# Kernel tuning notes

Hardware: AMD Instinct MI355X
Metric: run time of the kernel (lower is better)

Reference implementation:

```python
import jax, jax.numpy as jnp
import numpy as np

WS, SHIFT, HEADS, FEAT = 7, 3, 3, 56
N = WS * WS

def _rel_pos_index(ws):
    coords = np.stack(np.meshgrid(np.arange(ws), np.arange(ws), indexing='ij'))  # 2,ws,ws
    coords = coords.reshape(2, -1)
    rel = coords[:, :, None] - coords[:, None, :]            # 2,N,N
    rel = rel.transpose(1, 2, 0).astype(np.int64)            # N,N,2
    rel[:, :, 0] += ws - 1
    rel[:, :, 1] += ws - 1
    rel[:, :, 0] *= 2 * ws - 1
    return rel.sum(-1)                                       # N,N in [0,(2ws-1)^2)

def _shift_mask(H, ws, shift):
    img = np.zeros((H, H), dtype=np.float32)
    cnt = 0
    for hs in (slice(0, -ws), slice(-ws, -shift), slice(-shift, None)):
        for wl in (slice(0, -ws), slice(-ws, -shift), slice(-shift, None)):
            img[hs, wl] = cnt
            cnt += 1
    win = img.reshape(H // ws, ws, H // ws, ws).transpose(0, 2, 1, 3).reshape(-1, ws * ws)
    diff = win[:, None, :] - win[:, :, None]                 # nW,N,N (unsqueeze(1)-unsqueeze(2))
    return np.where(diff != 0, -100.0, 0.0).astype(np.float32)

_REL_IDX = jnp.asarray(_rel_pos_index(WS))
_MASK = jnp.asarray(_shift_mask(FEAT, WS, SHIFT))            # (nW_per_img, N, N)

def setup_inputs() -> dict:
    key = jax.random.key(0)
    ks = jax.random.split(key, 4)
    C = 96
    return {
        'x': jax.random.normal(ks[0], (128, C, FEAT, FEAT), jnp.float32),
        'ln_g': jnp.ones((C,), jnp.float32),
        'ln_b': jnp.zeros((C,), jnp.float32),
        'qkv_w': jax.random.normal(ks[1], (3 * C, C), jnp.float32) * 0.02,
        'qkv_b': jnp.zeros((3 * C,), jnp.float32),
        'proj_w': jax.random.normal(ks[2], (C, C), jnp.float32) * 0.02,
        'proj_b': jnp.zeros((C,), jnp.float32),
        'rel_table': jax.random.normal(ks[3], ((2 * WS - 1) ** 2, HEADS), jnp.float32) * 0.02,
    }

def reference(x, ln_g, ln_b, qkv_w, qkv_b, proj_w, proj_b, rel_table):
    B, C, H, W = x.shape
    hd = C // HEADS
    nwh = H // WS
    # BCHW -> BHWC, LayerNorm over C
    xt = x.transpose(0, 2, 3, 1)
    mu = xt.mean(-1, keepdims=True)
    var = ((xt - mu) ** 2).mean(-1, keepdims=True)
    xn = (xt - mu) * jax.lax.rsqrt(var + 1e-5) * ln_g + ln_b
    # cyclic shift
    xn = jnp.roll(xn, (-SHIFT, -SHIFT), axis=(1, 2))
    # window partition -> (B*nW, N, C)
    win = xn.reshape(B, nwh, WS, nwh, WS, C).transpose(0, 1, 3, 2, 4, 5).reshape(-1, N, C)
    # qkv
    qkv = (win @ qkv_w.T + qkv_b).reshape(-1, N, 3, HEADS, hd).transpose(2, 0, 3, 1, 4)
    q, k, v = qkv[0], qkv[1], qkv[2]                         # (B*nW, heads, N, hd)
    attn = jnp.einsum('whid,whjd->whij', q * (hd ** -0.5), k)
    bias = rel_table[_REL_IDX].transpose(2, 0, 1)            # heads,N,N
    attn = attn + bias[None]
    nWp = nwh * nwh
    attn = attn.reshape(B, nWp, HEADS, N, N) + _MASK[None, :, None]
    attn = jax.nn.softmax(attn, axis=-1).reshape(-1, HEADS, N, N)
    out = jnp.einsum('whij,whjd->whid', attn, v).transpose(0, 2, 1, 3).reshape(-1, N, C)
    out = out @ proj_w.T + proj_b
    # window reverse + unshift
    out = out.reshape(B, nwh, nwh, WS, WS, C).transpose(0, 1, 3, 2, 4, 5).reshape(B, H, W, C)
    out = jnp.roll(out, (SHIFT, SHIFT), axis=(1, 2))
    return out.transpose(0, 3, 1, 2)
```

## Files before the change

kernel.cpp:

```cpp
#include <hip/hip_runtime.h>

typedef unsigned short u16;
typedef __bf16 bf8v __attribute__((ext_vector_type(8)));
typedef float f4v __attribute__((ext_vector_type(4)));
typedef f4v __attribute__((may_alias)) f4va;
typedef unsigned int u2v __attribute__((ext_vector_type(2)));
typedef u2v __attribute__((may_alias)) u2va;
typedef unsigned int u4v __attribute__((ext_vector_type(4)));
typedef u4v __attribute__((may_alias)) u4va;

#define NTOK   49
#define NPAD   64
#define CDIM   96
#define FEAT_  56
#define HWIM   3136
#define SHIFT_ 3

#define WIN_ELEMS (128 * 64 * 49 * 96)
#define QW_ELEMS  (288 * 96)
#define PW_ELEMS  (96 * 96)
#define WS_NEEDED ((size_t)(WIN_ELEMS + QW_ELEMS + PW_ELEMS) * 2)

__device__ __forceinline__ float b2f(u16 u) {
  unsigned v = ((unsigned)u) << 16;
  return __builtin_bit_cast(float, v);
}
__device__ __forceinline__ u16 f2b(float f) {
  return __builtin_bit_cast(u16, (__bf16)f);
}
__device__ __forceinline__ unsigned pk2(float a, float b) {
  return (unsigned)f2b(a) | ((unsigned)f2b(b) << 16);
}
__device__ __forceinline__ bf8v fragld(const u16* p) {
  return __builtin_bit_cast(bf8v, *(const f4va*)p);
}
__device__ __forceinline__ bf8v cvt8(const float* p) {
  f4v a = *(const f4va*)p;
  f4v b = *(const f4va*)(p + 4);
  union { u16 u[8]; bf8v v; } r;
#pragma unroll
  for (int j = 0; j < 4; ++j) { r.u[j] = f2b(a[j]); r.u[4 + j] = f2b(b[j]); }
  return r.v;
}
__device__ __forceinline__ f4v mfma16(bf8v a, bf8v b, f4v c) {
  return __builtin_amdgcn_mfma_f32_16x16x32_bf16(a, b, c, 0, 0, 0);
}
__device__ __forceinline__ int reg3(int g) { return g < 49 ? 0 : (g < 53 ? 1 : 2); }

__global__ __launch_bounds__(256)
void swin_wcvt(const float* __restrict__ qw, const float* __restrict__ pw,
               u16* __restrict__ qwb, u16* __restrict__ pwb) {
  int i = blockIdx.x * 256 + threadIdx.x;
  if (i < QW_ELEMS) qwb[i] = f2b(qw[i]);
  else              pwb[i - QW_ELEMS] = f2b(pw[i - QW_ELEMS]);
}

__global__ __launch_bounds__(256, 6)
void swin_ln_pack(const float* __restrict__ x,
                  const float* __restrict__ lng, const float* __restrict__ lnb,
                  u16* __restrict__ winbuf) {
  __shared__ __align__(16) float xf[CDIM][60];
  __shared__ float ps[4][64], pq[4][64];
  __shared__ float gw[CDIM], bw[CDIM];

  const int bid = blockIdx.x;
  const int b = bid / FEAT_, hs = bid - b * FEAT_;
  int h = hs + SHIFT_; if (h >= FEAT_) h -= FEAT_;
  const int tid = threadIdx.x, wv = tid >> 6, lane = tid & 63;

  for (int i = tid; i < CDIM; i += 256) { gw[i] = lng[i]; bw[i] = lnb[i]; }

  const float* base = x + (size_t)b * CDIM * HWIM + h * FEAT_;
  for (int idx = tid; idx < 1344; idx += 256) {
    int c = idx / 14, p4 = idx - c * 14;
    *(f4va*)&xf[c][p4 * 4] = *(const f4va*)(base + (size_t)c * HWIM + p4 * 4);
  }
  __syncthreads();

  const int ws = lane;
  int wsrc = ws + SHIFT_; if (wsrc >= FEAT_) wsrc -= FEAT_;
  float s = 0.f, q = 0.f;
  if (ws < FEAT_)
    for (int i = 0; i < 24; ++i) {
      float v = xf[wv * 24 + i][wsrc];
      s += v; q += v * v;
    }
  ps[wv][lane] = s; pq[wv][lane] = q;
  __syncthreads();

  if (ws < FEAT_) {
    float ts = ps[0][ws] + ps[1][ws] + ps[2][ws] + ps[3][ws];
    float tq = pq[0][ws] + pq[1][ws] + pq[2][ws] + pq[3][ws];
    float m = ts * (1.f / 96.f);
    float r = rsqrtf(tq * (1.f / 96.f) - m * m + 1e-5f);
    const int ww = ws / 7, wl = ws - ww * 7;
    const int wrow = hs / 7, tr = hs - wrow * 7;
    u16* dst = winbuf + ((size_t)((b * 64 + wrow * 8 + ww) * 49 + tr * 7 + wl)) * CDIM + wv * 24;
    unsigned pkw[12];
#pragma unroll
    for (int i = 0; i < 12; ++i) {
      int c = wv * 24 + 2 * i;
      float v0 = (xf[c][wsrc] - m) * r * gw[c] + bw[c];
      float v1 = (xf[c + 1][wsrc] - m) * r * gw[c + 1] + bw[c + 1];
      pkw[i] = pk2(v0, v1);
    }
    u4v d0 = {pkw[0], pkw[1], pkw[2], pkw[3]};
    u4v d1 = {pkw[4], pkw[5], pkw[6], pkw[7]};
    u4v d2 = {pkw[8], pkw[9], pkw[10], pkw[11]};
    *(u4va*)(dst)      = d0;
    *(u4va*)(dst + 8)  = d1;
    *(u4va*)(dst + 16) = d2;
  }
}

__global__ __launch_bounds__(256, 3)
void swin_attn(u16* __restrict__ winbuf,
               const u16* __restrict__ qwb, const u16* __restrict__ pwb,
               const float* __restrict__ qbv, const float* __restrict__ pbv,
               const float* __restrict__ rel) {
  __shared__ __align__(16) u16 qk[NPAD][200];
  __shared__ __align__(16) u16 vt[3][32][72];
  __shared__ __align__(16) u16 Pl[NPAD][72];
  __shared__ float rel_f[507];
  __shared__ __align__(16) float pb_f[CDIM];
  __shared__ __align__(16) float qb_f[3 * CDIM];

  const int blk = blockIdx.x;
  const int wi = blk & 63;
  const int whb = wi >> 3, wwb = wi & 7;
  const int tid = threadIdx.x;
  const int wv = tid >> 6, lane = tid & 63;
  const int quad = lane >> 4, l15 = lane & 15;

  u16* wbase = winbuf + (size_t)blk * (NTOK * CDIM);

  for (int idx = tid; idx < 588; idx += 256) {
    int row = idx / 12, cc = idx - row * 12;
    *(f4va*)&qk[row][cc * 8] = *(const f4va*)(wbase + idx * 8);
  }
  {
    f4v z = {0.f, 0.f, 0.f, 0.f};
    for (int idx = tid; idx < 180; idx += 256) {
      int row = 49 + idx / 12, cc = idx - (idx / 12) * 12;
      *(f4va*)&qk[row][cc * 8] = z;
    }
  }
  for (int i = tid; i < 507; i += 256) rel_f[i] = rel[i];
  for (int i = tid; i < 3 * CDIM; i += 256) qb_f[i] = qbv[i];
  for (int i = tid; i < CDIM; i += 256) pb_f[i] = pbv[i];
  __syncthreads();

  {
    bf8v a[4][3];
#pragma unroll
    for (int mt = 0; mt < 4; ++mt)
#pragma unroll
      for (int kt = 0; kt < 3; ++kt)
        a[mt][kt] = fragld(&qk[mt * 16 + l15][kt * 32 + quad * 8]);
    __syncthreads();
    const float qscale = 0.17677669529663687f;
    for (int nt = wv; nt < 18; nt += 4) {
      int n = nt * 16 + l15;
      bf8v bf[3];
#pragma unroll
      for (int kt = 0; kt < 3; ++kt)
        bf[kt] = fragld(qwb + n * CDIM + kt * 32 + quad * 8);
      if (nt < 12) {
        const int n0 = nt * 16 + quad * 4;
        f4v bias = *(const f4va*)&qb_f[n0];
        const bool isq = (nt < 6);
#pragma unroll
        for (int mt = 0; mt < 4; ++mt) {
          f4v c = {0.f, 0.f, 0.f, 0.f};
          c = mfma16(bf[0], a[mt][0], c);
          c = mfma16(bf[1], a[mt][1], c);
          c = mfma16(bf[2], a[mt][2], c);
          float v0 = c[0] + bias[0], v1 = c[1] + bias[1];
          float v2 = c[2] + bias[2], v3 = c[3] + bias[3];
          if (isq) { v0 *= qscale; v1 *= qscale; v2 *= qscale; v3 *= qscale; }
          u2v d; d[0] = pk2(v0, v1); d[1] = pk2(v2, v3);
          *(u2va*)&qk[mt * 16 + l15][n0] = d;
        }
      } else {
        float bias = qb_f[n];
        const int hd = (n - 192) >> 5, dc = (n - 192) & 31;
#pragma unroll
        for (int mt = 0; mt < 4; ++mt) {
          f4v c = {0.f, 0.f, 0.f, 0.f};
          c = mfma16(a[mt][0], bf[0], c);
          c = mfma16(a[mt][1], bf[1], c);
          c = mfma16(a[mt][2], bf[2], c);
          u2v d; d[0] = pk2(c[0] + bias, c[1] + bias);
          d[1] = pk2(c[2] + bias, c[3] + bias);
          *(u2va*)&vt[hd][dc][mt * 16 + quad * 4] = d;
        }
      }
    }
  }
  __syncthreads();

  {
    const int mrow = wv * 16 + l15;
    int mc = mrow > 48 ? 48 : mrow;
    const int ri = mc / 7, ci = mc - ri * 7;
    const int rcnt = reg3(whb * 7 + ri) * 3 + reg3(wwb * 7 + ci);
    int ib_[4][4]; float ms_[4][4]; bool jv_[4][4];
#pragma unroll
    for (int jt = 0; jt < 4; ++jt)
#pragma unroll
      for (int rg = 0; rg < 4; ++rg) {
        int j = jt * 16 + quad * 4 + rg;
        jv_[jt][rg] = (j < NTOK);
        int jj = j > 48 ? 48 : j;
        int rj = jj / 7, cj = jj - rj * 7;
        int jcnt = reg3(whb * 7 + rj) * 3 + reg3(wwb * 7 + cj);
        ib_[jt][rg] = ((ri - rj + 6) * 13 + (ci - cj + 6)) * 3;
        ms_[jt][rg] = (jcnt != rcnt) ? -100.f : 0.f;
      }
#pragma unroll
    for (int h = 0; h < 3; ++h) {
      bf8v aq = fragld(&qk[wv * 16 + l15][h * 32 + quad * 8]);
      f4v S[4];
#pragma unroll
      for (int jt = 0; jt < 4; ++jt) {
        bf8v bk = fragld(&qk[jt * 16 + l15][96 + h * 32 + quad * 8]);
        f4v z = {0.f, 0.f, 0.f, 0.f};
        S[jt] = mfma16(bk, aq, z);
      }
#pragma unroll
      for (int jt = 0; jt < 4; ++jt)
#pragma unroll
        for (int rg = 0; rg < 4; ++rg) {
          if (jv_[jt][rg]) S[jt][rg] += rel_f[ib_[jt][rg] + h] + ms_[jt][rg];
          else             S[jt][rg] = -1e30f;
        }
      float mx0 = fmaxf(fmaxf(S[0][0], S[0][1]), fmaxf(S[0][2], S[0][3]));
      float mx1 = fmaxf(fmaxf(S[1][0], S[1][1]), fmaxf(S[1][2], S[1][3]));
      float mx2 = fmaxf(fmaxf(S[2][0], S[2][1]), fmaxf(S[2][2], S[2][3]));
      float mx3 = fmaxf(fmaxf(S[3][0], S[3][1]), fmaxf(S[3][2], S[3][3]));
      float mx = fmaxf(fmaxf(mx0, mx1), fmaxf(mx2, mx3));
      mx = fmaxf(mx, __shfl_xor(mx, 16, 64));
      mx = fmaxf(mx, __shfl_xor(mx, 32, 64));
      float s = 0.f;
#pragma unroll
      for (int jt = 0; jt < 4; ++jt) {
        float e0 = __expf(S[jt][0] - mx), e1 = __expf(S[jt][1] - mx);
        float e2 = __expf(S[jt][2] - mx), e3 = __expf(S[jt][3] - mx);
        S[jt][0] = e0; S[jt][1] = e1; S[jt][2] = e2; S[jt][3] = e3;
        s += (e0 + e1) + (e2 + e3);
      }
      s += __shfl_xor(s, 16, 64);
      s += __shfl_xor(s, 32, 64);
      float inv = 1.f / s;
#pragma unroll
      for (int jt = 0; jt < 4; ++jt) {
        u2v d; d[0] = pk2(S[jt][0] * inv, S[jt][1] * inv);
        d[1] = pk2(S[jt][2] * inv, S[jt][3] * inv);
        *(u2va*)&Pl[mrow][jt * 16 + quad * 4] = d;
      }
      bf8v ap0 = fragld(&Pl[wv * 16 + l15][quad * 8]);
      bf8v ap1 = fragld(&Pl[wv * 16 + l15][32 + quad * 8]);
#pragma unroll
      for (int dt = 0; dt < 2; ++dt) {
        bf8v bv0 = fragld(&vt[h][dt * 16 + l15][quad * 8]);
        bf8v bv1 = fragld(&vt[h][dt * 16 + l15][32 + quad * 8]);
        f4v c = {0.f, 0.f, 0.f, 0.f};
        c = mfma16(bv0, ap0, c);
        c = mfma16(bv1, ap1, c);
        u2v d; d[0] = pk2(c[0], c[1]); d[1] = pk2(c[2], c[3]);
        *(u2va*)&qk[mrow][h * 32 + dt * 16 + quad * 4] = d;
      }
    }
  }
  __syncthreads();

  {
    bf8v a[4][3];
#pragma unroll
    for (int mt = 0; mt < 4; ++mt)
#pragma unroll
      for (int kt = 0; kt < 3; ++kt)
        a[mt][kt] = fragld(&qk[mt * 16 + l15][kt * 32 + quad * 8]);
    __syncthreads();
    for (int nt = wv; nt < 6; nt += 4) {
      int n = nt * 16 + l15;
      bf8v bf[3];
#pragma unroll
      for (int kt = 0; kt < 3; ++kt)
        bf[kt] = fragld(pwb + n * CDIM + kt * 32 + quad * 8);
      const int n0 = nt * 16 + quad * 4;
      f4v bias = *(const f4va*)&pb_f[n0];
#pragma unroll
      for (int mt = 0; mt < 4; ++mt) {
        f4v c = {0.f, 0.f, 0.f, 0.f};
        c = mfma16(bf[0], a[mt][0], c);
        c = mfma16(bf[1], a[mt][1], c);
        c = mfma16(bf[2], a[mt][2], c);
        u2v d; d[0] = pk2(c[0] + bias[0], c[1] + bias[1]);
        d[1] = pk2(c[2] + bias[2], c[3] + bias[3]);
        *(u2va*)&qk[mt * 16 + l15][n0] = d;
      }
    }
  }
  __syncthreads();

  for (int idx = tid; idx < 588; idx += 256) {
    int row = idx / 12, cc = idx - row * 12;
    *(f4va*)(wbase + idx * 8) = *(const f4va*)&qk[row][cc * 8];
  }
}

__global__ __launch_bounds__(256, 8)
void swin_unpack(const u16* __restrict__ winbuf, float* __restrict__ out) {
  __shared__ __align__(16) u16 wtile[64][104];
  const int bid = blockIdx.x;
  const int b = bid / FEAT_, h = bid - b * FEAT_;
  int hs = h - SHIFT_; if (hs < 0) hs += FEAT_;
  const int wrow = hs / 7, tr = hs - wrow * 7;
  const int tid = threadIdx.x, wv = tid >> 6, lane = tid & 63;

  for (int idx = tid; idx < 672; idx += 256) {
    int ww = idx / 84, r = idx - ww * 84;
    const u16* src = winbuf + ((size_t)((b * 64 + wrow * 8 + ww) * 49 + tr * 7)) * CDIM + r * 8;
    int wl = r / 12, cc = r - wl * 12;
    int ws = ww * 7 + wl;
    int w = ws + SHIFT_; if (w >= FEAT_) w -= FEAT_;
    int sr = (w >> 2) | ((w & 3) << 4);
    *(f4va*)&wtile[sr][cc * 8] = *(const f4va*)src;
  }
  __syncthreads();
  if (lane < 56) {
    const int g = lane / 14, p4 = lane - g * 14;
    float* obase = out + (size_t)b * CDIM * HWIM + h * FEAT_ + p4 * 4;
    for (int i = 0; i < 6; ++i) {
      int c = wv * 24 + i * 4 + g;
      f4v v;
#pragma unroll
      for (int j = 0; j < 4; ++j) v[j] = b2f(wtile[p4 + 16 * j][c]);
      *(f4va*)(obase + (size_t)c * HWIM) = v;
    }
  }
}

__global__ __launch_bounds__(256, 2)
void swin_fused_fb(const float* __restrict__ x,
                   const float* __restrict__ lng, const float* __restrict__ lnb,
                   const float* __restrict__ qw,  const float* __restrict__ qbv,
                   const float* __restrict__ pw,  const float* __restrict__ pbv,
                   const float* __restrict__ rel,
                   float* __restrict__ out) {
  __shared__ union { float xf[NTOK][97]; u16 qk[NPAD][200]; } A;
  __shared__ union { u16 win16[NPAD][104]; u16 outb[NPAD][98]; } Bu;
  __shared__ u16 vt[3][32][72];
  __shared__ u16 Pl[NPAD][72];
  __shared__ u16 att[NPAD][104];
  __shared__ float gw[CDIM], bwt[CDIM];
  __shared__ float rel_f[507];
  __shared__ float pb_f[CDIM];
  __shared__ float qb_f[3 * CDIM];

  const int blk = blockIdx.x;
  const int b = blk >> 6, wi = blk & 63;
  const int whb = wi >> 3, wwb = wi & 7;
  const int tid = threadIdx.x, wv = tid >> 6, lane = tid & 63;
  const int quad = lane >> 4, l15 = lane & 15;
  {
    int p = lane;
    if (p < NTOK) {
      int r = p / 7, cw = p - r * 7;
      int h = whb * 7 + r + SHIFT_;  if (h >= FEAT_) h -= FEAT_;
      int w = wwb * 7 + cw + SHIFT_; if (w >= FEAT_) w -= FEAT_;
      const float* xp = x + b * CDIM * HWIM + h * FEAT_ + w;
      for (int c = wv; c < CDIM; c += 4) A.xf[p][c] = xp[c * HWIM];
    }
    for (int i = tid; i < CDIM; i += 256) { gw[i] = lng[i]; bwt[i] = lnb[i]; pb_f[i] = pbv[i]; }
    for (int i = tid; i < 507; i += 256) rel_f[i] = rel[i];
    for (int i = tid; i < 3 * CDIM; i += 256) qb_f[i] = qbv[i];
  }
  __syncthreads();
  {
    int p = wv * 16 + (lane >> 2), cg = lane & 3;
    float s = 0.f, q = 0.f;
    if (p < NTOK)
      for (int i = 0; i < 24; ++i) { float v = A.xf[p][cg * 24 + i]; s += v; q += v * v; }
    s += __shfl_xor(s, 1, 64); s += __shfl_xor(s, 2, 64);
    q += __shfl_xor(q, 1, 64); q += __shfl_xor(q, 2, 64);
    float m = s * (1.f / 96.f);
    float r = rsqrtf(q * (1.f / 96.f) - m * m + 1e-5f);
    for (int i = 0; i < 24; ++i) {
      int c = cg * 24 + i;
      float v = (p < NTOK) ? (A.xf[p][c] - m) * r * gw[c] + bwt[c] : 0.f;
      Bu.win16[p][c] = f2b(v);
    }
  }
  __syncthreads();
  {
    bf8v a[4][3];
    for (int mt = 0; mt < 4; ++mt)
      for (int kt = 0; kt < 3; ++kt)
        a[mt][kt] = fragld(&Bu.win16[mt * 16 + l15][kt * 32 + quad * 8]);
    const float qscale = 0.17677669529663687f;
    for (int nt = wv; nt < 18; nt += 4) {
      int n = nt * 16 + l15;
      const float* wr = qw + n * CDIM;
      bf8v bf[3];
      for (int kt = 0; kt < 3; ++kt) bf[kt] = cvt8(wr + kt * 32 + quad * 8);
      float bias = qb_f[n];
      for (int mt = 0; mt < 4; ++mt) {
        f4v c = {0.f, 0.f, 0.f, 0.f};
        c = mfma16(a[mt][0], bf[0], c);
        c = mfma16(a[mt][1], bf[1], c);
        c = mfma16(a[mt][2], bf[2], c);
        for (int rg = 0; rg < 4; ++rg) {
          int m = mt * 16 + quad * 4 + rg;
          float v = c[rg] + bias;
          if (n < 96)        A.qk[m][n] = f2b(v * qscale);
          else if (n < 192)  A.qk[m][n] = f2b(v);
          else               vt[(n - 192) >> 5][(n - 192) & 31][m] = f2b(v);
        }
      }
    }
  }
  __syncthreads();
  {
    const int rbase = wv * 16 + quad * 4;
    int rcnt[4], ri_[4], ci_[4];
    for (int rg = 0; rg < 4; ++rg) {
      int r = rbase + rg; if (r > 48) r = 48;
      int ri = r / 7, ci = r - ri * 7;
      ri_[rg] = ri; ci_[rg] = ci;
      rcnt[rg] = reg3(whb * 7 + ri) * 3 + reg3(wwb * 7 + ci);
    }
    for (int h = 0; h < 3; ++h) {
      bf8v aq = fragld(&A.qk[wv * 16 + l15][h * 32 + quad * 8]);
      f4v S[4];
      for (int nt = 0; nt < 4; ++nt) {
        bf8v bk = fragld(&A.qk[nt * 16 + l15][96 + h * 32 + quad * 8]);
        f4v z = {0.f, 0.f, 0.f, 0.f};
        S[nt] = mfma16(aq, bk, z);
      }
      for (int nt = 0; nt < 4; ++nt) {
        int j = nt * 16 + l15;
        if (j < NTOK) {
          int rj = j / 7, cj = j - rj * 7;
          int jcnt = reg3(whb * 7 + rj) * 3 + reg3(wwb * 7 + cj);
          for (int rg = 0; rg < 4; ++rg) {
            float add = rel_f[((ri_[rg] - rj + 6) * 13 + (ci_[rg] - cj + 6)) * 3 + h];
            if (jcnt != rcnt[rg]) add -= 100.f;
            S[nt][rg] += add;
          }
        } else {
          for (int rg = 0; rg < 4; ++rg) S[nt][rg] = -1e30f;
        }
      }
      float inv[4];
      for (int rg = 0; rg < 4; ++rg) {
        float m = fmaxf(fmaxf(S[0][rg], S[1][rg]), fmaxf(S[2][rg], S[3][rg]));
        for (int off = 1; off < 16; off <<= 1) m = fmaxf(m, __shfl_xor(m, off, 64));
        float s = 0.f;
        for (int nt = 0; nt < 4; ++nt) { float e = __expf(S[nt][rg] - m); S[nt][rg] = e; s += e; }
        for (int off = 1; off < 16; off <<= 1) s += __shfl_xor(s, off, 64);
        inv[rg] = 1.f / s;
      }
      for (int nt = 0; nt < 4; ++nt) {
        int j = nt * 16 + l15;
        for (int rg = 0; rg < 4; ++rg) Pl[rbase + rg][j] = f2b(S[nt][rg] * inv[rg]);
      }
      bf8v ap0 = fragld(&Pl[wv * 16 + l15][quad * 8]);
      bf8v ap1 = fragld(&Pl[wv * 16 + l15][32 + quad * 8]);
      for (int nt = 0; nt < 2; ++nt) {
        bf8v bv0 = fragld(&vt[h][nt * 16 + l15][quad * 8]);
        bf8v bv1 = fragld(&vt[h][nt * 16 + l15][32 + quad * 8]);
        f4v c = {0.f, 0.f, 0.f, 0.f};
        c = mfma16(ap0, bv0, c);
        c = mfma16(ap1, bv1, c);
        for (int rg = 0; rg < 4; ++rg)
          att[rbase + rg][h * 32 + nt * 16 + l15] = f2b(c[rg]);
      }
    }
  }
  __syncthreads();
  {
    bf8v a[4][3];
    for (int mt = 0; mt < 4; ++mt)
      for (int kt = 0; kt < 3; ++kt)
        a[mt][kt] = fragld(&att[mt * 16 + l15][kt * 32 + quad * 8]);
    for (int nt = wv; nt < 6; nt += 4) {
      int n = nt * 16 + l15;
      const float* wr = pw + n * CDIM;
      bf8v bf[3];
      for (int kt = 0; kt < 3; ++kt) bf[kt] = cvt8(wr + kt * 32 + quad * 8);
      float bias = pb_f[n];
      for (int mt = 0; mt < 4; ++mt) {
        f4v c = {0.f, 0.f, 0.f, 0.f};
        c = mfma16(a[mt][0], bf[0], c);
        c = mfma16(a[mt][1], bf[1], c);
        c = mfma16(a[mt][2], bf[2], c);
        for (int rg = 0; rg < 4; ++rg)
          Bu.outb[mt * 16 + quad * 4 + rg][n] = f2b(c[rg] + bias);
      }
    }
  }
  __syncthreads();
  {
    int p = lane;
    if (p < NTOK) {
      int r = p / 7, cw = p - r * 7;
      int h = whb * 7 + r + SHIFT_;  if (h >= FEAT_) h -= FEAT_;
      int w = wwb * 7 + cw + SHIFT_; if (w >= FEAT_) w -= FEAT_;
      float* op = out + b * CDIM * HWIM + h * FEAT_ + w;
      for (int c = wv; c < CDIM; c += 4) op[c * HWIM] = b2f(Bu.outb[p][c]);
    }
  }
}

extern "C" void kernel_launch(void* const* d_in, const int* in_sizes, int n_in,
                              void* d_out, int out_size, void* d_ws, size_t ws_size,
                              hipStream_t stream) {
  (void)in_sizes; (void)n_in; (void)out_size;
  const float* x   = (const float*)d_in[0];
  const float* lng = (const float*)d_in[1];
  const float* lnb = (const float*)d_in[2];
  const float* qw  = (const float*)d_in[3];
  const float* qbv = (const float*)d_in[4];
  const float* pw  = (const float*)d_in[5];
  const float* pbv = (const float*)d_in[6];
  const float* rel = (const float*)d_in[7];
  float* out = (float*)d_out;

  if (ws_size >= WS_NEEDED) {
    u16* winbuf = (u16*)d_ws;
    u16* qwb = winbuf + WIN_ELEMS;
    u16* pwb = qwb + QW_ELEMS;
    swin_wcvt<<<dim3(144), dim3(256), 0, stream>>>(qw, pw, qwb, pwb);
    swin_ln_pack<<<dim3(128 * FEAT_), dim3(256), 0, stream>>>(x, lng, lnb, winbuf);
    swin_attn<<<dim3(8192), dim3(256), 0, stream>>>(winbuf, qwb, pwb, qbv, pbv, rel);
    swin_unpack<<<dim3(128 * FEAT_), dim3(256), 0, stream>>>(winbuf, out);
  } else {
    swin_fused_fb<<<dim3(8192), dim3(256), 0, stream>>>(x, lng, lnb, qw, qbv, pw, pbv, rel, out);
  }
}
```

Baseline: 447.7 us.

## Fuse layernorm pack, window attention and unpack into one kernel

```diff
diff --git a/kernel.cpp b/kernel.cpp
--- a/kernel.cpp
+++ b/kernel.cpp
@@ -16,10 +16,9 @@
 #define HWIM   3136
 #define SHIFT_ 3
 
-#define WIN_ELEMS (128 * 64 * 49 * 96)
 #define QW_ELEMS  (288 * 96)
 #define PW_ELEMS  (96 * 96)
-#define WS_NEEDED ((size_t)(WIN_ELEMS + QW_ELEMS + PW_ELEMS) * 2)
+#define WS_NEEDED ((size_t)(QW_ELEMS + PW_ELEMS) * 2)
 
 __device__ __forceinline__ float b2f(u16 u) {
   unsigned v = ((unsigned)u) << 16;
@@ -55,99 +54,77 @@
   else              pwb[i - QW_ELEMS] = f2b(pw[i - QW_ELEMS]);
 }
 
-__global__ __launch_bounds__(256, 6)
-void swin_ln_pack(const float* __restrict__ x,
-                  const float* __restrict__ lng, const float* __restrict__ lnb,
-                  u16* __restrict__ winbuf) {
-  __shared__ __align__(16) float xf[CDIM][60];
-  __shared__ float ps[4][64], pq[4][64];
+__global__ __launch_bounds__(256, 3)
+void swin_mono(const float* __restrict__ x,
+               const float* __restrict__ lng, const float* __restrict__ lnb,
+               const u16* __restrict__ qwb, const u16* __restrict__ pwb,
+               const float* __restrict__ qbv, const float* __restrict__ pbv,
+               const float* __restrict__ rel, float* __restrict__ out) {
+  __shared__ __align__(16) u16 qk[NPAD][200];
+  __shared__ __align__(16) union {
+    struct { u16 vt[3][32][72]; u16 Pl[NPAD][72]; } s;
+    float xf[NTOK][97];
+  } U;
+  __shared__ float rel_f[507];
+  __shared__ __align__(16) float pb_f[CDIM];
+  __shared__ __align__(16) float qb_f[3 * CDIM];
   __shared__ float gw[CDIM], bw[CDIM];
 
   const int bid = blockIdx.x;
-  const int b = bid / FEAT_, hs = bid - b * FEAT_;
-  int h = hs + SHIFT_; if (h >= FEAT_) h -= FEAT_;
-  const int tid = threadIdx.x, wv = tid >> 6, lane = tid & 63;
-
-  for (int i = tid; i < CDIM; i += 256) { gw[i] = lng[i]; bw[i] = lnb[i]; }
-
-  const float* base = x + (size_t)b * CDIM * HWIM + h * FEAT_;
-  for (int idx = tid; idx < 1344; idx += 256) {
-    int c = idx / 14, p4 = idx - c * 14;
-    *(f4va*)&xf[c][p4 * 4] = *(const f4va*)(base + (size_t)c * HWIM + p4 * 4);
-  }
-  __syncthreads();
-
-  const int ws = lane;
-  int wsrc = ws + SHIFT_; if (wsrc >= FEAT_) wsrc -= FEAT_;
-  float s = 0.f, q = 0.f;
-  if (ws < FEAT_)
-    for (int i = 0; i < 24; ++i) {
-      float v = xf[wv * 24 + i][wsrc];
-      s += v; q += v * v;
-    }
-  ps[wv][lane] = s; pq[wv][lane] = q;
-  __syncthreads();
-
-  if (ws < FEAT_) {
-    float ts = ps[0][ws] + ps[1][ws] + ps[2][ws] + ps[3][ws];
-    float tq = pq[0][ws] + pq[1][ws] + pq[2][ws] + pq[3][ws];
-    float m = ts * (1.f / 96.f);
-    float r = rsqrtf(tq * (1.f / 96.f) - m * m + 1e-5f);
-    const int ww = ws / 7, wl = ws - ww * 7;
-    const int wrow = hs / 7, tr = hs - wrow * 7;
-    u16* dst = winbuf + ((size_t)((b * 64 + wrow * 8 + ww) * 49 + tr * 7 + wl)) * CDIM + wv * 24;
+  const int wwb = bid >> 10;
+  const int b = (bid >> 3) & 127;
+  const int whb = bid & 7;
+  const int tid = threadIdx.x;
+  const int wv = tid >> 6, lane = tid & 63;
+  const int quad = lane >> 4, l15 = lane & 15;
+
+  for (int i = tid; i < 507; i += 256) rel_f[i] = rel[i];
+  for (int i = tid; i < 3 * CDIM; i += 256) qb_f[i] = qbv[i];
+  for (int i = tid; i < CDIM; i += 256) { pb_f[i] = pbv[i]; gw[i] = lng[i]; bw[i] = lnb[i]; }
+
+  const int w0 = wwb * 7 + SHIFT_;
+  for (int idx = tid; idx < 672; idx += 256) {
+    int r = idx / 96, c = idx - r * 96;
+    int hsrc = whb * 7 + r + SHIFT_; if (hsrc >= FEAT_) hsrc -= FEAT_;
+    const float* xp = x + ((size_t)b * CDIM + c) * HWIM + hsrc * FEAT_;
+#pragma unroll
+    for (int wl = 0; wl < 7; ++wl) {
+      int wsrc = w0 + wl; if (wsrc >= FEAT_) wsrc -= FEAT_;
+      U.xf[r * 7 + wl][c] = xp[wsrc];
+    }
+  }
+  __syncthreads();
+
+  {
+    const int p = tid >> 2, cg = tid & 3;
+    const float* xr = U.xf[p < NTOK ? p : 0];
+    float s = 0.f, q = 0.f;
+    if (p < NTOK)
+#pragma unroll
+      for (int i = 0; i < 24; ++i) { float v = xr[cg * 24 + i]; s += v; q += v * v; }
+    s += __shfl_xor(s, 1, 64); s += __shfl_xor(s, 2, 64);
+    q += __shfl_xor(q, 1, 64); q += __shfl_xor(q, 2, 64);
+    float m = s * (1.f / 96.f);
+    float r = rsqrtf(q * (1.f / 96.f) - m * m + 1e-5f);
     unsigned pkw[12];
 #pragma unroll
     for (int i = 0; i < 12; ++i) {
-      int c = wv * 24 + 2 * i;
-      float v0 = (xf[c][wsrc] - m) * r * gw[c] + bw[c];
-      float v1 = (xf[c + 1][wsrc] - m) * r * gw[c + 1] + bw[c + 1];
+      int c0 = cg * 24 + 2 * i;
+      float v0 = 0.f, v1 = 0.f;
+      if (p < NTOK) {
+        v0 = (xr[c0] - m) * r * gw[c0] + bw[c0];
+        v1 = (xr[c0 + 1] - m) * r * gw[c0 + 1] + bw[c0 + 1];
+      }
       pkw[i] = pk2(v0, v1);
     }
     u4v d0 = {pkw[0], pkw[1], pkw[2], pkw[3]};
     u4v d1 = {pkw[4], pkw[5], pkw[6], pkw[7]};
     u4v d2 = {pkw[8], pkw[9], pkw[10], pkw[11]};
+    u16* dst = &qk[p][cg * 24];
     *(u4va*)(dst)      = d0;
     *(u4va*)(dst + 8)  = d1;
     *(u4va*)(dst + 16) = d2;
   }
-}
-
-__global__ __launch_bounds__(256, 3)
-void swin_attn(u16* __restrict__ winbuf,
-               const u16* __restrict__ qwb, const u16* __restrict__ pwb,
-               const float* __restrict__ qbv, const float* __restrict__ pbv,
-               const float* __restrict__ rel) {
-  __shared__ __align__(16) u16 qk[NPAD][200];
-  __shared__ __align__(16) u16 vt[3][32][72];
-  __shared__ __align__(16) u16 Pl[NPAD][72];
-  __shared__ float rel_f[507];
-  __shared__ __align__(16) float pb_f[CDIM];
-  __shared__ __align__(16) float qb_f[3 * CDIM];
-
-  const int blk = blockIdx.x;
-  const int wi = blk & 63;
-  const int whb = wi >> 3, wwb = wi & 7;
-  const int tid = threadIdx.x;
-  const int wv = tid >> 6, lane = tid & 63;
-  const int quad = lane >> 4, l15 = lane & 15;
-
-  u16* wbase = winbuf + (size_t)blk * (NTOK * CDIM);
-
-  for (int idx = tid; idx < 588; idx += 256) {
-    int row = idx / 12, cc = idx - row * 12;
-    *(f4va*)&qk[row][cc * 8] = *(const f4va*)(wbase + idx * 8);
-  }
-  {
-    f4v z = {0.f, 0.f, 0.f, 0.f};
-    for (int idx = tid; idx < 180; idx += 256) {
-      int row = 49 + idx / 12, cc = idx - (idx / 12) * 12;
-      *(f4va*)&qk[row][cc * 8] = z;
-    }
-  }
-  for (int i = tid; i < 507; i += 256) rel_f[i] = rel[i];
-  for (int i = tid; i < 3 * CDIM; i += 256) qb_f[i] = qbv[i];
-  for (int i = tid; i < CDIM; i += 256) pb_f[i] = pbv[i];
   __syncthreads();
 
   {
@@ -192,7 +169,7 @@
           c = mfma16(a[mt][2], bf[2], c);
           u2v d; d[0] = pk2(c[0] + bias, c[1] + bias);
           d[1] = pk2(c[2] + bias, c[3] + bias);
-          *(u2va*)&vt[hd][dc][mt * 16 + quad * 4] = d;
+          *(u2va*)&U.s.vt[hd][dc][mt * 16 + quad * 4] = d;
         }
       }
     }
@@ -256,14 +233,14 @@
       for (int jt = 0; jt < 4; ++jt) {
         u2v d; d[0] = pk2(S[jt][0] * inv, S[jt][1] * inv);
         d[1] = pk2(S[jt][2] * inv, S[jt][3] * inv);
-        *(u2va*)&Pl[mrow][jt * 16 + quad * 4] = d;
-      }
-      bf8v ap0 = fragld(&Pl[wv * 16 + l15][quad * 8]);
-      bf8v ap1 = fragld(&Pl[wv * 16 + l15][32 + quad * 8]);
+        *(u2va*)&U.s.Pl[mrow][jt * 16 + quad * 4] = d;
+      }
+      bf8v ap0 = fragld(&U.s.Pl[wv * 16 + l15][quad * 8]);
+      bf8v ap1 = fragld(&U.s.Pl[wv * 16 + l15][32 + quad * 8]);
 #pragma unroll
       for (int dt = 0; dt < 2; ++dt) {
-        bf8v bv0 = fragld(&vt[h][dt * 16 + l15][quad * 8]);
-        bf8v bv1 = fragld(&vt[h][dt * 16 + l15][32 + quad * 8]);
+        bf8v bv0 = fragld(&U.s.vt[h][dt * 16 + l15][quad * 8]);
+        bf8v bv1 = fragld(&U.s.vt[h][dt * 16 + l15][32 + quad * 8]);
         f4v c = {0.f, 0.f, 0.f, 0.f};
         c = mfma16(bv0, ap0, c);
         c = mfma16(bv1, ap1, c);
@@ -304,40 +281,14 @@
   }
   __syncthreads();
 
-  for (int idx = tid; idx < 588; idx += 256) {
-    int row = idx / 12, cc = idx - row * 12;
-    *(f4va*)(wbase + idx * 8) = *(const f4va*)&qk[row][cc * 8];
-  }
-}
-
-__global__ __launch_bounds__(256, 8)
-void swin_unpack(const u16* __restrict__ winbuf, float* __restrict__ out) {
-  __shared__ __align__(16) u16 wtile[64][104];
-  const int bid = blockIdx.x;
-  const int b = bid / FEAT_, h = bid - b * FEAT_;
-  int hs = h - SHIFT_; if (hs < 0) hs += FEAT_;
-  const int wrow = hs / 7, tr = hs - wrow * 7;
-  const int tid = threadIdx.x, wv = tid >> 6, lane = tid & 63;
-
   for (int idx = tid; idx < 672; idx += 256) {
-    int ww = idx / 84, r = idx - ww * 84;
-    const u16* src = winbuf + ((size_t)((b * 64 + wrow * 8 + ww) * 49 + tr * 7)) * CDIM + r * 8;
-    int wl = r / 12, cc = r - wl * 12;
-    int ws = ww * 7 + wl;
-    int w = ws + SHIFT_; if (w >= FEAT_) w -= FEAT_;
-    int sr = (w >> 2) | ((w & 3) << 4);
-    *(f4va*)&wtile[sr][cc * 8] = *(const f4va*)src;
-  }
-  __syncthreads();
-  if (lane < 56) {
-    const int g = lane / 14, p4 = lane - g * 14;
-    float* obase = out + (size_t)b * CDIM * HWIM + h * FEAT_ + p4 * 4;
-    for (int i = 0; i < 6; ++i) {
-      int c = wv * 24 + i * 4 + g;
-      f4v v;
-#pragma unroll
-      for (int j = 0; j < 4; ++j) v[j] = b2f(wtile[p4 + 16 * j][c]);
-      *(f4va*)(obase + (size_t)c * HWIM) = v;
+    int r = idx / 96, c = idx - r * 96;
+    int hdst = whb * 7 + r + SHIFT_; if (hdst >= FEAT_) hdst -= FEAT_;
+    float* op = out + ((size_t)b * CDIM + c) * HWIM + hdst * FEAT_;
+#pragma unroll
+    for (int wl = 0; wl < 7; ++wl) {
+      int wdst = w0 + wl; if (wdst >= FEAT_) wdst -= FEAT_;
+      op[wdst] = b2f(qk[r * 7 + wl][c]);
     }
   }
 }
@@ -529,13 +480,10 @@
   float* out = (float*)d_out;
 
   if (ws_size >= WS_NEEDED) {
-    u16* winbuf = (u16*)d_ws;
-    u16* qwb = winbuf + WIN_ELEMS;
+    u16* qwb = (u16*)d_ws;
     u16* pwb = qwb + QW_ELEMS;
     swin_wcvt<<<dim3(144), dim3(256), 0, stream>>>(qw, pw, qwb, pwb);
-    swin_ln_pack<<<dim3(128 * FEAT_), dim3(256), 0, stream>>>(x, lng, lnb, winbuf);
-    swin_attn<<<dim3(8192), dim3(256), 0, stream>>>(winbuf, qwb, pwb, qbv, pbv, rel);
-    swin_unpack<<<dim3(128 * FEAT_), dim3(256), 0, stream>>>(winbuf, out);
+    swin_mono<<<dim3(8192), dim3(256), 0, stream>>>(x, lng, lnb, qwb, pwb, qbv, pbv, rel, out);
   } else {
     swin_fused_fb<<<dim3(8192), dim3(256), 0, stream>>>(x, lng, lnb, qw, qbv, pw, pbv, rel, out);
   }
```

Result: slower. 581.5 us (+29.9%).
